# Kernel optimization log

Hardware: AMD Instinct MI355X
Metric: run time of the kernel (lower is better)

## Reference

```python
import jax, jax.numpy as jnp
import numpy as np

N = 100_000      # nodes
E = 1_600_000    # edges (avg degree 16)
D = 64           # input_dim
H = 64           # hidden_dim
G = 2048         # graphs in batch
EPS = 1e-5       # BatchNorm eps


def setup_inputs() -> dict:
    key = jax.random.key(0)
    ks = jax.random.split(key, 12)
    x = jax.random.normal(ks[0], (N, D), dtype=jnp.float32)
    edge_index = jax.random.randint(ks[1], (2, E), 0, N, dtype=jnp.int64)
    batch = jnp.sort(jax.random.randint(ks[2], (N,), 0, G, dtype=jnp.int64))
    s = 1.0 / np.sqrt(D)
    W1 = jax.random.normal(ks[3], (D, H), dtype=jnp.float32) * s
    b1 = jnp.zeros((H,), jnp.float32)
    g1 = jnp.ones((H,), jnp.float32)
    bt1 = jnp.zeros((H,), jnp.float32)
    W2 = jax.random.normal(ks[4], (H, H), dtype=jnp.float32) * s
    b2 = jnp.zeros((H,), jnp.float32)
    g2 = jnp.ones((H,), jnp.float32)
    bt2 = jnp.zeros((H,), jnp.float32)
    return {"x": x, "edge_index": edge_index, "batch": batch,
            "W1": W1, "b1": b1, "g1": g1, "bt1": bt1,
            "W2": W2, "b2": b2, "g2": g2, "bt2": bt2,
            "num_graphs": G}


def reference(x, edge_index, batch, W1, b1, g1, bt1, W2, b2, g2, bt2, num_graphs):
    n = x.shape[0]
    # GCN normalization with added self-loops (PyG GCNConv default)
    loops = jnp.arange(n, dtype=edge_index.dtype)
    src = jnp.concatenate([edge_index[0], loops])
    dst = jnp.concatenate([edge_index[1], loops])
    deg = jax.ops.segment_sum(jnp.ones(src.shape, jnp.float32), dst, num_segments=n)
    dis = jax.lax.rsqrt(jnp.maximum(deg, 1.0))  # deg >= 1 with self-loops
    norm = dis[src] * dis[dst]                  # [E+N]

    def gcn(h, W, b):
        h = h @ W                               # [N,H] dense transform first
        msg = h[src] * norm[:, None]            # gather + scale  [E+N, H]
        return jax.ops.segment_sum(msg, dst, num_segments=n) + b

    def bn(h, gamma, beta):
        mu = h.mean(axis=0)
        var = h.var(axis=0)
        return (h - mu) * jax.lax.rsqrt(var + EPS) * gamma + beta

    h = jax.nn.relu(bn(gcn(x, W1, b1), g1, bt1))
    h = jax.nn.relu(bn(gcn(h, W2, b2), g2, bt2))

    # global mean pool over graph ids
    ones = jnp.ones((n,), jnp.float32)
    counts = jax.ops.segment_sum(ones, batch, num_segments=num_graphs)
    sums = jax.ops.segment_sum(h, batch, num_segments=num_graphs)
    return sums / jnp.maximum(counts, 1.0)[:, None]
```

## Files before the change

kernel.cpp:

```cpp
#include <hip/hip_runtime.h>
#include <hip/hip_bf16.h>

#define BN_EPS 1e-5f
#define CCHUNK 16384

__device__ __forceinline__ ushort f2bf(float f) {
    unsigned int u = __float_as_uint(f);
    u += 0x7FFFu + ((u >> 16) & 1u);
    return (ushort)(u >> 16);
}

__global__ void k_bhist(const int* __restrict__ dst, int E, int nb, int* __restrict__ bktcnt,
                        const int* __restrict__ batch, int n, int G, int* __restrict__ gs) {
    int gid = blockIdx.x * blockDim.x + threadIdx.x;
    if (gid <= G) {
        int lo = 0, hi = n;
        while (lo < hi) { int mid = (lo + hi) >> 1; if (batch[mid] < gid) lo = mid + 1; else hi = mid; }
        gs[gid] = lo;
    }
    __shared__ int lh[1024];
    for (int j = threadIdx.x; j < nb; j += 256) lh[j] = 0;
    __syncthreads();
    for (int i = blockIdx.x * blockDim.x + threadIdx.x; i < E; i += gridDim.x * blockDim.x)
        atomicAdd(&lh[dst[i] >> 7], 1);
    __syncthreads();
    for (int j = threadIdx.x; j < nb; j += 256) {
        int c = lh[j];
        if (c) atomicAdd(&bktcnt[j], c);
    }
}

__global__ void k_bscan(const int* __restrict__ bktcnt, int nb, int N,
                        int* __restrict__ bktoff, int* __restrict__ gpos,
                        int* __restrict__ rowptr) {
    __shared__ int sh[256];
    int tid = threadIdx.x;
    int base = tid * 4;
    int v[4]; int tsum = 0;
    #pragma unroll
    for (int k = 0; k < 4; ++k) {
        int i = base + k;
        v[k] = (i < nb) ? bktcnt[i] : 0;
        tsum += v[k];
    }
    sh[tid] = tsum;
    __syncthreads();
    for (int off = 1; off < 256; off <<= 1) {
        int add = (tid >= off) ? sh[tid - off] : 0;
        __syncthreads();
        sh[tid] += add;
        __syncthreads();
    }
    int excl = sh[tid] - tsum;
    #pragma unroll
    for (int k = 0; k < 4; ++k) {
        int i = base + k;
        if (i <= nb) {
            bktoff[i] = excl;
            if (i < nb) gpos[i] = excl;
        }
        excl += v[k];
    }
    if (tid == 255) rowptr[N] = sh[255];
}

__global__ void k_partition(const int* __restrict__ src, const int* __restrict__ dst,
                            int E, int nb, int sb,
                            int* __restrict__ gpos, unsigned int* __restrict__ eb) {
    __shared__ int lh[1024];
    int e0 = blockIdx.x * CCHUNK;
    int cnt = min(CCHUNK, E - e0);
    for (int j = threadIdx.x; j < nb; j += 256) lh[j] = 0;
    __syncthreads();
    for (int k = threadIdx.x; k < cnt; k += 256)
        atomicAdd(&lh[dst[e0 + k] >> 7], 1);
    __syncthreads();
    for (int j = threadIdx.x; j < nb; j += 256) {
        int c = lh[j];
        if (c) lh[j] = atomicAdd(&gpos[j], c);
    }
    __syncthreads();
    for (int k = threadIdx.x; k < cnt; k += 256) {
        int d = dst[e0 + k];
        unsigned int s = (unsigned int)src[e0 + k];
        int pos = atomicAdd(&lh[d >> 7], 1);
        eb[pos] = (((unsigned int)(d & 127)) << sb) | s;
    }
}

__global__ void k_row(const unsigned int* __restrict__ eb, const int* __restrict__ bktoff,
                      int sb, int N, float* __restrict__ dis, int* __restrict__ rowptr) {
    __shared__ int h[128];
    __shared__ int p[128];
    int tid = threadIdx.x;
    int b = blockIdx.x;
    if (tid < 128) h[tid] = 0;
    __syncthreads();
    int e0 = bktoff[b], e1 = bktoff[b + 1];
    for (int e = e0 + tid; e < e1; e += 256)
        atomicAdd(&h[(eb[e] >> sb) & 127], 1);
    __syncthreads();
    if (tid < 128) p[tid] = h[tid];
    __syncthreads();
    for (int off = 1; off < 128; off <<= 1) {
        int add = (tid < 128 && tid >= off) ? p[tid - off] : 0;
        __syncthreads();
        if (tid < 128) p[tid] += add;
        __syncthreads();
    }
    if (tid < 128) {
        int d = b * 128 + tid;
        if (d < N) {
            rowptr[d] = e0 + p[tid] - h[tid];
            dis[d] = rsqrtf((float)(h[tid] + 1));
        }
    }
}

__global__ void k_csrfill(const unsigned int* __restrict__ eb, const int* __restrict__ bktoff,
                          const int* __restrict__ rowptr, const float* __restrict__ dis,
                          int sb, unsigned int smask, int N, int2* __restrict__ cw) {
    __shared__ int nc[128];
    __shared__ float dl[128];
    int tid = threadIdx.x;
    int b = blockIdx.x;
    if (tid < 128) {
        int d = b * 128 + tid;
        nc[tid] = (d < N) ? rowptr[d] : 0;
        dl[tid] = (d < N) ? dis[d] : 1.f;
    }
    __syncthreads();
    int e0 = bktoff[b], e1 = bktoff[b + 1];
    for (int e = e0 + tid; e < e1; e += 256) {
        unsigned int v = eb[e];
        int dloc = (v >> sb) & 127;
        int s = (int)(v & smask);
        int slot = atomicAdd(&nc[dloc], 1);
        cw[slot] = make_int2(s, __float_as_int(dis[s] * dl[dloc]));
    }
}

__global__ void k_matmul64t(const float* __restrict__ X, const float* __restrict__ W,
                            const float* __restrict__ stats, const float* __restrict__ gamma,
                            const float* __restrict__ beta, int n, ushort* __restrict__ tb) {
    __shared__ float Xs[64][68];
    __shared__ float Ws[64][64];
    __shared__ float bnpL[128];
    const int tid = threadIdx.x;
    const int rowbase = blockIdx.x * 64;
    const bool hasbn = (stats != nullptr);

    {
        const float4* W4 = (const float4*)W;
        float4* Ws4 = (float4*)&Ws[0][0];
        #pragma unroll
        for (int k = 0; k < 4; ++k) Ws4[tid + 256 * k] = W4[tid + 256 * k];
    }
    if (hasbn) {
        if (tid < 64) {
            float inv_n = 1.f / (float)n;
            float mean = stats[tid] * inv_n;
            float var = stats[64 + tid] * inv_n - mean * mean;
            float s = gamma[tid] * rsqrtf(var + BN_EPS);
            bnpL[tid] = s;
            bnpL[64 + tid] = beta[tid] - mean * s;
        }
        __syncthreads();
    }
    {
        const int r  = tid >> 2;
        const int c0 = (tid & 3) * 16;
        const int row = rowbase + r;
        #pragma unroll
        for (int j = 0; j < 4; ++j) {
            float4 v;
            if (row < n) v = *(const float4*)&X[(size_t)row * 64 + c0 + 4 * j];
            else v = make_float4(0.f, 0.f, 0.f, 0.f);
            float vv[4] = {v.x, v.y, v.z, v.w};
            #pragma unroll
            for (int i = 0; i < 4; ++i) {
                int c = c0 + 4 * j + i;
                float f = vv[i];
                if (hasbn) f = fmaxf(0.f, fmaf(f, bnpL[c], bnpL[64 + c]));
                Xs[c][r] = f;
            }
        }
    }
    __syncthreads();

    const int r0 = (tid & 15) * 4;
    const int c0 = (tid >> 4) * 4;
    float acc[4][4];
    #pragma unroll
    for (int i = 0; i < 4; ++i)
        #pragma unroll
        for (int j = 0; j < 4; ++j) acc[i][j] = 0.f;

    #pragma unroll 4
    for (int k = 0; k < 64; ++k) {
        float4 xv = *(const float4*)&Xs[k][r0];
        float4 wv = *(const float4*)&Ws[k][c0];
        float xa[4] = {xv.x, xv.y, xv.z, xv.w};
        float wa[4] = {wv.x, wv.y, wv.z, wv.w};
        #pragma unroll
        for (int i = 0; i < 4; ++i)
            #pragma unroll
            for (int j = 0; j < 4; ++j)
                acc[i][j] = fmaf(xa[i], wa[j], acc[i][j]);
    }

    #pragma unroll
    for (int i = 0; i < 4; ++i) {
        int row = rowbase + r0 + i;
        if (row < n) {
            ushort4 o;
            o.x = f2bf(acc[i][0]); o.y = f2bf(acc[i][1]);
            o.z = f2bf(acc[i][2]); o.w = f2bf(acc[i][3]);
            *(ushort4*)&tb[(size_t)row * 64 + c0] = o;
        }
    }
}

__global__ void k_gather(const int2* __restrict__ cw, const int* __restrict__ rowptr,
                         const float* __restrict__ dis, const ushort* __restrict__ tb,
                         int n, float* __restrict__ a, float* __restrict__ stats) {
    __shared__ float ls[128];
    int tid = threadIdx.x;
    if (tid < 128) ls[tid] = 0.f;
    __syncthreads();
    int lane = tid & 63;
    int wave = tid >> 6;
    const int fl = lane & 7;
    const int o  = lane >> 3;
    float psum[8], psq[8];
    #pragma unroll
    for (int i = 0; i < 8; ++i) { psum[i] = 0.f; psq[i] = 0.f; }

    for (int row = blockIdx.x * 4 + wave; row < n; row += gridDim.x * 4) {
        int e0 = rowptr[row], e1 = rowptr[row + 1];
        float acc[8];
        #pragma unroll
        for (int i = 0; i < 8; ++i) acc[i] = 0.f;
        for (int base = e0; base < e1; base += 64) {
            int cnt = min(64, e1 - base);
            int2 pw = (lane < cnt) ? cw[base + lane] : make_int2(0, 0);
            int nq = (cnt + 7) >> 3;
            for (int j = 0; j < nq; ++j) {
                int idx = 8 * j + o;
                int s = __shfl(pw.x, idx);
                float w = __uint_as_float((unsigned int)__shfl(pw.y, idx));
                uint4 tv = *(const uint4*)&tb[(size_t)s * 64 + 8 * fl];
                acc[0] = fmaf(__uint_as_float(tv.x << 16),         w, acc[0]);
                acc[1] = fmaf(__uint_as_float(tv.x & 0xffff0000u), w, acc[1]);
                acc[2] = fmaf(__uint_as_float(tv.y << 16),         w, acc[2]);
                acc[3] = fmaf(__uint_as_float(tv.y & 0xffff0000u), w, acc[3]);
                acc[4] = fmaf(__uint_as_float(tv.z << 16),         w, acc[4]);
                acc[5] = fmaf(__uint_as_float(tv.z & 0xffff0000u), w, acc[5]);
                acc[6] = fmaf(__uint_as_float(tv.w << 16),         w, acc[6]);
                acc[7] = fmaf(__uint_as_float(tv.w & 0xffff0000u), w, acc[7]);
            }
        }
        #pragma unroll
        for (int i = 0; i < 8; ++i) {
            acc[i] += __shfl_xor(acc[i], 8);
            acc[i] += __shfl_xor(acc[i], 16);
            acc[i] += __shfl_xor(acc[i], 32);
        }
        if (o == 0) {
            float dr = dis[row];
            float d2 = dr * dr;
            uint4 ts = *(const uint4*)&tb[(size_t)row * 64 + 8 * fl];
            acc[0] = fmaf(__uint_as_float(ts.x << 16),         d2, acc[0]);
            acc[1] = fmaf(__uint_as_float(ts.x & 0xffff0000u), d2, acc[1]);
            acc[2] = fmaf(__uint_as_float(ts.y << 16),         d2, acc[2]);
            acc[3] = fmaf(__uint_as_float(ts.y & 0xffff0000u), d2, acc[3]);
            acc[4] = fmaf(__uint_as_float(ts.z << 16),         d2, acc[4]);
            acc[5] = fmaf(__uint_as_float(ts.z & 0xffff0000u), d2, acc[5]);
            acc[6] = fmaf(__uint_as_float(ts.w << 16),         d2, acc[6]);
            acc[7] = fmaf(__uint_as_float(ts.w & 0xffff0000u), d2, acc[7]);
            *(float4*)&a[(size_t)row * 64 + 8 * fl]     = make_float4(acc[0], acc[1], acc[2], acc[3]);
            *(float4*)&a[(size_t)row * 64 + 8 * fl + 4] = make_float4(acc[4], acc[5], acc[6], acc[7]);
            #pragma unroll
            for (int i = 0; i < 8; ++i) {
                psum[i] += acc[i];
                psq[i] = fmaf(acc[i], acc[i], psq[i]);
            }
        }
    }
    if (o == 0) {
        #pragma unroll
        for (int i = 0; i < 8; ++i) {
            atomicAdd(&ls[8 * fl + i], psum[i]);
            atomicAdd(&ls[64 + 8 * fl + i], psq[i]);
        }
    }
    __syncthreads();
    if (tid < 128) atomicAdd(&stats[tid], ls[tid]);
}

__global__ void k_pool2(const float* __restrict__ a, const float* __restrict__ stats,
                        const float* __restrict__ gamma, const float* __restrict__ beta,
                        const int* __restrict__ gs, int n, int G, float* __restrict__ out) {
    __shared__ float bnpL[128];
    int tid = threadIdx.x;
    if (tid < 64) {
        float inv_n = 1.f / (float)n;
        float mean = stats[tid] * inv_n;
        float var = stats[64 + tid] * inv_n - mean * mean;
        float s = gamma[tid] * rsqrtf(var + BN_EPS);
        bnpL[tid] = s;
        bnpL[64 + tid] = beta[tid] - mean * s;
    }
    __syncthreads();
    int lane = tid & 63;
    int wave = tid >> 6;
    int g = blockIdx.x * 4 + wave;
    if (g >= G) return;
    int s = gs[g], e = gs[g + 1];
    float sc = bnpL[lane], of = bnpL[64 + lane];
    float acc = 0.f;
    for (int r = s; r < e; ++r)
        acc += fmaxf(0.f, fmaf(a[(size_t)r * 64 + lane], sc, of));
    out[(size_t)g * 64 + lane] = acc / (float)max(e - s, 1);
}

extern "C" void kernel_launch(void* const* d_in, const int* in_sizes, int n_in,
                              void* d_out, int out_size, void* d_ws, size_t ws_size,
                              hipStream_t stream) {
    const float* x     = (const float*)d_in[0];
    const int*   ei    = (const int*)d_in[1];
    const int*   batch = (const int*)d_in[2];
    const float* W1    = (const float*)d_in[3];
    const float* g1    = (const float*)d_in[5];
    const float* bt1   = (const float*)d_in[6];
    const float* W2    = (const float*)d_in[7];
    const float* g2    = (const float*)d_in[9];
    const float* bt2   = (const float*)d_in[10];

    const int N = in_sizes[0] / 64;
    const int E = in_sizes[1] / 2;
    const int G = out_size / 64;

    const int* src = ei;
    const int* dst = ei + E;

    const int nb = (N + 127) >> 7;
    int sb = 0; while ((1 << sb) < N) ++sb;
    const unsigned int smask = (1u << sb) - 1u;

    ushort* tb        = (ushort*)d_ws;
    float* a          = (float*)(tb + (size_t)N * 64);
    int2*  cw         = (int2*)(a + (size_t)N * 64);
    unsigned int* eb  = (unsigned int*)(cw + E);
    float* dis        = (float*)(eb + E);
    int*   rowptr     = (int*)(dis + N);
    int*   bktcnt     = rowptr + N + 1;
    float* stats      = (float*)(bktcnt + nb);
    int*   bktoff     = (int*)(stats + 256);
    int*   gpos       = bktoff + nb + 1;
    int*   gs         = gpos + nb;

    float* out = (float*)d_out;

    const int mmBlocks = (N + 63) / 64;
    const int gaBlocks = 2048;
    const int pcBlocks = (E + CCHUNK - 1) / CCHUNK;

    hipMemsetAsync(bktcnt, 0, (size_t)(nb + 256) * sizeof(int), stream);
    k_bhist<<<256, 256, 0, stream>>>(dst, E, nb, bktcnt, batch, N, G, gs);
    k_bscan<<<1, 256, 0, stream>>>(bktcnt, nb, N, bktoff, gpos, rowptr);
    k_partition<<<pcBlocks, 256, 0, stream>>>(src, dst, E, nb, sb, gpos, eb);
    k_row<<<nb, 256, 0, stream>>>(eb, bktoff, sb, N, dis, rowptr);
    k_csrfill<<<nb, 256, 0, stream>>>(eb, bktoff, rowptr, dis, sb, smask, N, cw);

    k_matmul64t<<<mmBlocks, 256, 0, stream>>>(x, W1, nullptr, nullptr, nullptr, N, tb);
    k_gather<<<gaBlocks, 256, 0, stream>>>(cw, rowptr, dis, tb, N, a, stats);

    k_matmul64t<<<mmBlocks, 256, 0, stream>>>(a, W2, stats, g1, bt1, N, tb);
    k_gather<<<gaBlocks, 256, 0, stream>>>(cw, rowptr, dis, tb, N, a, stats + 128);

    k_pool2<<<(G + 3) / 4, 256, 0, stream>>>(a, stats + 128, g2, bt2, gs, N, G, out);
}
```

Before: 352.5 us.

## Launch one gather block per four rows and reduce BN stats via slotted scratch

The gather kernel now launches one block per four rows instead of a fixed grid-stride over 2048 blocks, so each wave handles exactly one row. Per-block BatchNorm statistics are accumulated into 256 scratch slots with atomics instead of a single global array, and a small follow-up kernel sums the slots. This aims to balance irregular row work across many small blocks and to avoid global atomic contention. In exchange it adds per-row shared atomics, 25k block launches, two extra kernel launches and a larger memset.

```diff
diff --git a/kernel.cpp b/kernel.cpp
--- a/kernel.cpp
+++ b/kernel.cpp
@@ -3,6 +3,7 @@
 
 #define BN_EPS 1e-5f
 #define CCHUNK 16384
+#define NSLOT 256
 
 __device__ __forceinline__ ushort f2bf(float f) {
     unsigned int u = __float_as_uint(f);
@@ -223,7 +224,7 @@
 
 __global__ void k_gather(const int2* __restrict__ cw, const int* __restrict__ rowptr,
                          const float* __restrict__ dis, const ushort* __restrict__ tb,
-                         int n, float* __restrict__ a, float* __restrict__ stats) {
+                         int n, float* __restrict__ a, float* __restrict__ sscr) {
     __shared__ float ls[128];
     int tid = threadIdx.x;
     if (tid < 128) ls[tid] = 0.f;
@@ -232,11 +233,8 @@
     int wave = tid >> 6;
     const int fl = lane & 7;
     const int o  = lane >> 3;
-    float psum[8], psq[8];
-    #pragma unroll
-    for (int i = 0; i < 8; ++i) { psum[i] = 0.f; psq[i] = 0.f; }
-
-    for (int row = blockIdx.x * 4 + wave; row < n; row += gridDim.x * 4) {
+    int row = blockIdx.x * 4 + wave;
+    if (row < n) {
         int e0 = rowptr[row], e1 = rowptr[row + 1];
         float acc[8];
         #pragma unroll
@@ -282,20 +280,23 @@
             *(float4*)&a[(size_t)row * 64 + 8 * fl + 4] = make_float4(acc[4], acc[5], acc[6], acc[7]);
             #pragma unroll
             for (int i = 0; i < 8; ++i) {
-                psum[i] += acc[i];
-                psq[i] = fmaf(acc[i], acc[i], psq[i]);
+                atomicAdd(&ls[8 * fl + i], acc[i]);
+                atomicAdd(&ls[64 + 8 * fl + i], acc[i] * acc[i]);
             }
         }
     }
-    if (o == 0) {
-        #pragma unroll
-        for (int i = 0; i < 8; ++i) {
-            atomicAdd(&ls[8 * fl + i], psum[i]);
-            atomicAdd(&ls[64 + 8 * fl + i], psq[i]);
-        }
-    }
-    __syncthreads();
-    if (tid < 128) atomicAdd(&stats[tid], ls[tid]);
+    __syncthreads();
+    if (tid < 128)
+        atomicAdd(&sscr[(size_t)(blockIdx.x & (NSLOT - 1)) * 128 + tid], ls[tid]);
+}
+
+__global__ void k_statsred(const float* __restrict__ sscr, float* __restrict__ stats) {
+    int c = threadIdx.x;
+    float s = 0.f;
+    #pragma unroll 8
+    for (int k = 0; k < NSLOT; ++k)
+        s += sscr[(size_t)k * 128 + c];
+    stats[c] = s;
 }
 
 __global__ void k_pool2(const float* __restrict__ a, const float* __restrict__ stats,
@@ -356,17 +357,18 @@
     int*   rowptr     = (int*)(dis + N);
     int*   bktcnt     = rowptr + N + 1;
     float* stats      = (float*)(bktcnt + nb);
-    int*   bktoff     = (int*)(stats + 256);
+    float* sscr       = stats + 256;
+    int*   bktoff     = (int*)(sscr + 2 * NSLOT * 128);
     int*   gpos       = bktoff + nb + 1;
     int*   gs         = gpos + nb;
 
     float* out = (float*)d_out;
 
     const int mmBlocks = (N + 63) / 64;
-    const int gaBlocks = 2048;
+    const int gaBlocks = (N + 3) / 4;
     const int pcBlocks = (E + CCHUNK - 1) / CCHUNK;
 
-    hipMemsetAsync(bktcnt, 0, (size_t)(nb + 256) * sizeof(int), stream);
+    hipMemsetAsync(bktcnt, 0, (size_t)(nb + 256 + 2 * NSLOT * 128) * sizeof(int), stream);
     k_bhist<<<256, 256, 0, stream>>>(dst, E, nb, bktcnt, batch, N, G, gs);
     k_bscan<<<1, 256, 0, stream>>>(bktcnt, nb, N, bktoff, gpos, rowptr);
     k_partition<<<pcBlocks, 256, 0, stream>>>(src, dst, E, nb, sb, gpos, eb);
@@ -374,10 +376,12 @@
     k_csrfill<<<nb, 256, 0, stream>>>(eb, bktoff, rowptr, dis, sb, smask, N, cw);
 
     k_matmul64t<<<mmBlocks, 256, 0, stream>>>(x, W1, nullptr, nullptr, nullptr, N, tb);
-    k_gather<<<gaBlocks, 256, 0, stream>>>(cw, rowptr, dis, tb, N, a, stats);
+    k_gather<<<gaBlocks, 256, 0, stream>>>(cw, rowptr, dis, tb, N, a, sscr);
+    k_statsred<<<1, 128, 0, stream>>>(sscr, stats);
 
     k_matmul64t<<<mmBlocks, 256, 0, stream>>>(a, W2, stats, g1, bt1, N, tb);
-    k_gather<<<gaBlocks, 256, 0, stream>>>(cw, rowptr, dis, tb, N, a, stats + 128);
+    k_gather<<<gaBlocks, 256, 0, stream>>>(cw, rowptr, dis, tb, N, a, sscr + NSLOT * 128);
+    k_statsred<<<1, 128, 0, stream>>>(sscr + NSLOT * 128, stats + 128);
 
     k_pool2<<<(G + 3) / 4, 256, 0, stream>>>(a, stats + 128, g2, bt2, gs, N, G, out);
 }
```

New measurement: 379.1 us. +7.5%, slower.

## Split BN stats out of gather and launch one wave per row

Applied to the files above, without the earlier changes.

The gather kernel no longer loops over rows grid-stride with 2048 blocks. It now launches one block per four rows, with one wave per row and early exit, and drops the per-block shared-memory BatchNorm statistics accumulation. A separate k_stats kernel rereads the aggregated activations to compute per-channel sum and sum of squares. The goal is better load balance and latency hiding in the gather. The cost is two extra kernel launches and an extra pass over the 25.6MB activation buffer per layer.

```diff
diff --git a/kernel.cpp b/kernel.cpp
--- a/kernel.cpp
+++ b/kernel.cpp
@@ -223,76 +223,79 @@
 
 __global__ void k_gather(const int2* __restrict__ cw, const int* __restrict__ rowptr,
                          const float* __restrict__ dis, const ushort* __restrict__ tb,
-                         int n, float* __restrict__ a, float* __restrict__ stats) {
-    __shared__ float ls[128];
-    int tid = threadIdx.x;
-    if (tid < 128) ls[tid] = 0.f;
-    __syncthreads();
-    int lane = tid & 63;
-    int wave = tid >> 6;
+                         int n, float* __restrict__ a) {
+    int lane = threadIdx.x & 63;
+    int wave = threadIdx.x >> 6;
+    int row = blockIdx.x * 4 + wave;
+    if (row >= n) return;
     const int fl = lane & 7;
     const int o  = lane >> 3;
-    float psum[8], psq[8];
-    #pragma unroll
-    for (int i = 0; i < 8; ++i) { psum[i] = 0.f; psq[i] = 0.f; }
-
-    for (int row = blockIdx.x * 4 + wave; row < n; row += gridDim.x * 4) {
-        int e0 = rowptr[row], e1 = rowptr[row + 1];
-        float acc[8];
-        #pragma unroll
-        for (int i = 0; i < 8; ++i) acc[i] = 0.f;
-        for (int base = e0; base < e1; base += 64) {
-            int cnt = min(64, e1 - base);
-            int2 pw = (lane < cnt) ? cw[base + lane] : make_int2(0, 0);
-            int nq = (cnt + 7) >> 3;
-            for (int j = 0; j < nq; ++j) {
-                int idx = 8 * j + o;
-                int s = __shfl(pw.x, idx);
-                float w = __uint_as_float((unsigned int)__shfl(pw.y, idx));
-                uint4 tv = *(const uint4*)&tb[(size_t)s * 64 + 8 * fl];
-                acc[0] = fmaf(__uint_as_float(tv.x << 16),         w, acc[0]);
-                acc[1] = fmaf(__uint_as_float(tv.x & 0xffff0000u), w, acc[1]);
-                acc[2] = fmaf(__uint_as_float(tv.y << 16),         w, acc[2]);
-                acc[3] = fmaf(__uint_as_float(tv.y & 0xffff0000u), w, acc[3]);
-                acc[4] = fmaf(__uint_as_float(tv.z << 16),         w, acc[4]);
-                acc[5] = fmaf(__uint_as_float(tv.z & 0xffff0000u), w, acc[5]);
-                acc[6] = fmaf(__uint_as_float(tv.w << 16),         w, acc[6]);
-                acc[7] = fmaf(__uint_as_float(tv.w & 0xffff0000u), w, acc[7]);
-            }
-        }
-        #pragma unroll
-        for (int i = 0; i < 8; ++i) {
-            acc[i] += __shfl_xor(acc[i], 8);
-            acc[i] += __shfl_xor(acc[i], 16);
-            acc[i] += __shfl_xor(acc[i], 32);
-        }
-        if (o == 0) {
-            float dr = dis[row];
-            float d2 = dr * dr;
-            uint4 ts = *(const uint4*)&tb[(size_t)row * 64 + 8 * fl];
-            acc[0] = fmaf(__uint_as_float(ts.x << 16),         d2, acc[0]);
-            acc[1] = fmaf(__uint_as_float(ts.x & 0xffff0000u), d2, acc[1]);
-            acc[2] = fmaf(__uint_as_float(ts.y << 16),         d2, acc[2]);
-            acc[3] = fmaf(__uint_as_float(ts.y & 0xffff0000u), d2, acc[3]);
-            acc[4] = fmaf(__uint_as_float(ts.z << 16),         d2, acc[4]);
-            acc[5] = fmaf(__uint_as_float(ts.z & 0xffff0000u), d2, acc[5]);
-            acc[6] = fmaf(__uint_as_float(ts.w << 16),         d2, acc[6]);
-            acc[7] = fmaf(__uint_as_float(ts.w & 0xffff0000u), d2, acc[7]);
-            *(float4*)&a[(size_t)row * 64 + 8 * fl]     = make_float4(acc[0], acc[1], acc[2], acc[3]);
-            *(float4*)&a[(size_t)row * 64 + 8 * fl + 4] = make_float4(acc[4], acc[5], acc[6], acc[7]);
-            #pragma unroll
-            for (int i = 0; i < 8; ++i) {
-                psum[i] += acc[i];
-                psq[i] = fmaf(acc[i], acc[i], psq[i]);
-            }
-        }
+    int e0 = rowptr[row], e1 = rowptr[row + 1];
+    float acc[8];
+    #pragma unroll
+    for (int i = 0; i < 8; ++i) acc[i] = 0.f;
+    for (int base = e0; base < e1; base += 64) {
+        int cnt = min(64, e1 - base);
+        int2 pw = (lane < cnt) ? cw[base + lane] : make_int2(0, 0);
+        int nq = (cnt + 7) >> 3;
+        for (int j = 0; j < nq; ++j) {
+            int idx = 8 * j + o;
+            int s = __shfl(pw.x, idx);
+            float w = __uint_as_float((unsigned int)__shfl(pw.y, idx));
+            uint4 tv = *(const uint4*)&tb[(size_t)s * 64 + 8 * fl];
+            acc[0] = fmaf(__uint_as_float(tv.x << 16),         w, acc[0]);
+            acc[1] = fmaf(__uint_as_float(tv.x & 0xffff0000u), w, acc[1]);
+            acc[2] = fmaf(__uint_as_float(tv.y << 16),         w, acc[2]);
+            acc[3] = fmaf(__uint_as_float(tv.y & 0xffff0000u), w, acc[3]);
+            acc[4] = fmaf(__uint_as_float(tv.z << 16),         w, acc[4]);
+            acc[5] = fmaf(__uint_as_float(tv.z & 0xffff0000u), w, acc[5]);
+            acc[6] = fmaf(__uint_as_float(tv.w << 16),         w, acc[6]);
+            acc[7] = fmaf(__uint_as_float(tv.w & 0xffff0000u), w, acc[7]);
+        }
+    }
+    #pragma unroll
+    for (int i = 0; i < 8; ++i) {
+        acc[i] += __shfl_xor(acc[i], 8);
+        acc[i] += __shfl_xor(acc[i], 16);
+        acc[i] += __shfl_xor(acc[i], 32);
     }
     if (o == 0) {
-        #pragma unroll
-        for (int i = 0; i < 8; ++i) {
-            atomicAdd(&ls[8 * fl + i], psum[i]);
-            atomicAdd(&ls[64 + 8 * fl + i], psq[i]);
-        }
+        float dr = dis[row];
+        float d2 = dr * dr;
+        uint4 ts = *(const uint4*)&tb[(size_t)row * 64 + 8 * fl];
+        acc[0] = fmaf(__uint_as_float(ts.x << 16),         d2, acc[0]);
+        acc[1] = fmaf(__uint_as_float(ts.x & 0xffff0000u), d2, acc[1]);
+        acc[2] = fmaf(__uint_as_float(ts.y << 16),         d2, acc[2]);
+        acc[3] = fmaf(__uint_as_float(ts.y & 0xffff0000u), d2, acc[3]);
+        acc[4] = fmaf(__uint_as_float(ts.z << 16),         d2, acc[4]);
+        acc[5] = fmaf(__uint_as_float(ts.z & 0xffff0000u), d2, acc[5]);
+        acc[6] = fmaf(__uint_as_float(ts.w << 16),         d2, acc[6]);
+        acc[7] = fmaf(__uint_as_float(ts.w & 0xffff0000u), d2, acc[7]);
+        *(float4*)&a[(size_t)row * 64 + 8 * fl]     = make_float4(acc[0], acc[1], acc[2], acc[3]);
+        *(float4*)&a[(size_t)row * 64 + 8 * fl + 4] = make_float4(acc[4], acc[5], acc[6], acc[7]);
+    }
+}
+
+__global__ void k_stats(const float* __restrict__ a, int n, float* __restrict__ stats) {
+    __shared__ float ls[128];
+    int tid = threadIdx.x;
+    if (tid < 128) ls[tid] = 0.f;
+    __syncthreads();
+    int c0 = (tid & 15) * 4;
+    int rg = tid >> 4;
+    float s[4] = {0.f, 0.f, 0.f, 0.f};
+    float q[4] = {0.f, 0.f, 0.f, 0.f};
+    for (int r = blockIdx.x * 16 + rg; r < n; r += gridDim.x * 16) {
+        float4 v = *(const float4*)&a[(size_t)r * 64 + c0];
+        s[0] += v.x; q[0] = fmaf(v.x, v.x, q[0]);
+        s[1] += v.y; q[1] = fmaf(v.y, v.y, q[1]);
+        s[2] += v.z; q[2] = fmaf(v.z, v.z, q[2]);
+        s[3] += v.w; q[3] = fmaf(v.w, v.w, q[3]);
+    }
+    #pragma unroll
+    for (int i = 0; i < 4; ++i) {
+        atomicAdd(&ls[c0 + i], s[i]);
+        atomicAdd(&ls[64 + c0 + i], q[i]);
     }
     __syncthreads();
     if (tid < 128) atomicAdd(&stats[tid], ls[tid]);
@@ -363,7 +366,7 @@
     float* out = (float*)d_out;
 
     const int mmBlocks = (N + 63) / 64;
-    const int gaBlocks = 2048;
+    const int gaBlocks = (N + 3) / 4;
     const int pcBlocks = (E + CCHUNK - 1) / CCHUNK;
 
     hipMemsetAsync(bktcnt, 0, (size_t)(nb + 256) * sizeof(int), stream);
@@ -374,10 +377,12 @@
     k_csrfill<<<nb, 256, 0, stream>>>(eb, bktoff, rowptr, dis, sb, smask, N, cw);
 
     k_matmul64t<<<mmBlocks, 256, 0, stream>>>(x, W1, nullptr, nullptr, nullptr, N, tb);
-    k_gather<<<gaBlocks, 256, 0, stream>>>(cw, rowptr, dis, tb, N, a, stats);
+    k_gather<<<gaBlocks, 256, 0, stream>>>(cw, rowptr, dis, tb, N, a);
+    k_stats<<<512, 256, 0, stream>>>(a, N, stats);
 
     k_matmul64t<<<mmBlocks, 256, 0, stream>>>(a, W2, stats, g1, bt1, N, tb);
-    k_gather<<<gaBlocks, 256, 0, stream>>>(cw, rowptr, dis, tb, N, a, stats + 128);
+    k_gather<<<gaBlocks, 256, 0, stream>>>(cw, rowptr, dis, tb, N, a);
+    k_stats<<<512, 256, 0, stream>>>(a, N, stats + 128);
 
     k_pool2<<<(G + 3) / 4, 256, 0, stream>>>(a, stats + 128, g2, bt2, gs, N, G, out);
 }
```

After: 290.9 us. 1.21x faster.
